# Optimization experiments

Hardware: AMD Instinct MI355X
Metric: run time of the kernel (lower is better)

Reference implementation:

```python
import jax, jax.numpy as jnp
import numpy as np

N_USERS = 100_000
N_ITEMS = 50_000
N_NODES = N_USERS + N_ITEMS      # 150_000
EMB_DIM = 64
N_EDGES = 2_400_000              # avg degree ~16
N_LAYERS = 3
S_TEMP = 1.0                     # config['s_temp']


def segment_softmax(logits, seg, n):
    # numerically stable scatter-softmax over groups defined by seg
    m = jax.ops.segment_max(logits, seg, num_segments=n)
    e = jnp.exp(logits - m[seg])
    s = jax.ops.segment_sum(e, seg, num_segments=n)
    return e / s[seg]


def setup_inputs() -> dict:
    key = jax.random.key(0)
    k1, k2, k3 = jax.random.split(key, 3)
    emb_table = jax.random.normal(k1, (N_NODES, EMB_DIM), dtype=jnp.float32) * 0.1
    edge_index = jax.random.randint(k2, (2, N_EDGES), 0, N_NODES, dtype=jnp.int64)
    edge_attrs = jax.random.normal(k3, (N_EDGES,), dtype=jnp.float32)
    return {"emb_table": emb_table, "edge_index": edge_index, "edge_attrs": edge_attrs}


def reference(emb_table, edge_index, edge_attrs):
    frm, to = edge_index[0], edge_index[1]
    # DySimGCF edge normalization: geometric mean of incoming/outgoing scatter-softmax
    incoming = segment_softmax(edge_attrs / S_TEMP, to, N_NODES)
    outgoing = segment_softmax(edge_attrs / S_TEMP, frm, N_NODES)
    norm = jnp.sqrt(incoming * outgoing)          # [E]

    x = emb_table                                  # [N, D]
    embs = [x]
    for _ in range(N_LAYERS):
        # message = norm * x_j ; aggregate 'add' at destination == sparse mm
        msg = norm[:, None] * x[frm]               # [E, D]
        x = jax.ops.segment_sum(msg, to, num_segments=N_NODES)
        embs.append(x)
    # layer-average (lightGCN-style readout)
    out = jnp.mean(jnp.stack(embs, axis=1), axis=1)  # [N, D]
    return out
```

## Files before the change

### kernel.cpp

```cpp
#include <hip/hip_runtime.h>
#include <hip/hip_bf16.h>

#define N_NODES 150000
#define N_EDGES 2400000
#define DIM     64
#define MAXDEG  64

#define NB      256
#define NPB     587
#define NSHARD  4
#define CAPS    2816
#define BINBLK  512
#define BINTHR  512
#define EPB     ((N_EDGES + BINBLK - 1) / BINBLK)

__device__ __forceinline__ unsigned enc14(float v) {
    unsigned b = __float_as_uint(v);
    b += (1u << 13);
    int e5 = (int)((b >> 23) & 0xFF) - 104;
    if (e5 <= 0) return 0u;
    if (e5 > 31) e5 = 31;
    return ((unsigned)e5 << 9) | ((b >> 14) & 0x1FFu);
}
__device__ __forceinline__ float dec14(unsigned w) {
    return __uint_as_float((w << 14) + (104u << 23));
}
__device__ __forceinline__ unsigned packbf(float a, float b) {
    unsigned ua = __float_as_uint(a), ub = __float_as_uint(b);
    ua += 0x7FFFu + ((ua >> 16) & 1u);
    ub += 0x7FFFu + ((ub >> 16) & 1u);
    return (ua >> 16) | (ub & 0xFFFF0000u);
}
__device__ __forceinline__ float bflo(unsigned v) { return __uint_as_float(v << 16); }
__device__ __forceinline__ float bfhi(unsigned v) { return __uint_as_float(v & 0xFFFF0000u); }

__device__ __forceinline__ void scanNB(unsigned* scanBuf, int tid) {
    for (int off = 1; off < NB; off <<= 1) {
        unsigned v = 0u;
        if (tid < NB) { v = scanBuf[tid]; if (tid >= off) v += scanBuf[tid - off]; }
        __syncthreads();
        if (tid < NB) scanBuf[tid] = v;
        __syncthreads();
    }
}

__global__ __launch_bounds__(BINTHR) void binA_kernel(const float* __restrict__ attrs,
                                                      const int* __restrict__ frm,
                                                      const int* __restrict__ to,
                                                      unsigned* __restrict__ gcntT,
                                                      unsigned* __restrict__ gcntF,
                                                      uint2* __restrict__ recT,
                                                      unsigned* __restrict__ recF) {
    __shared__ unsigned hist[NB], baseL[NB], gBase[NB], cur[NB], scanBuf[NB];
    __shared__ uint2 bufT[EPB];
    unsigned* bufF = (unsigned*)bufT;

    int tid = threadIdx.x;
    int e0 = blockIdx.x * EPB;
    int e1 = e0 + EPB; if (e1 > N_EDGES) e1 = N_EDGES;
    int n = e1 - e0;
    unsigned shard = blockIdx.x & (NSHARD - 1);

    for (int i = tid; i < NB; i += BINTHR) { hist[i] = 0u; cur[i] = 0u; }
    __syncthreads();
    for (int e = e0 + tid; e < e1; e += BINTHR)
        atomicAdd(&hist[(unsigned)to[e] / NPB], 1u);
    __syncthreads();
    if (tid < NB) scanBuf[tid] = hist[tid];
    __syncthreads();
    scanNB(scanBuf, tid);
    if (tid < NB) {
        baseL[tid] = scanBuf[tid] - hist[tid];
        gBase[tid] = hist[tid] ? atomicAdd(&gcntT[tid * NSHARD + shard], hist[tid]) : 0u;
    }
    __syncthreads();
    for (int e = e0 + tid; e < e1; e += BINTHR) {
        unsigned t = (unsigned)to[e], f = (unsigned)frm[e];
        unsigned v14 = enc14(expf(attrs[e]));
        unsigned b = t / NPB;
        unsigned pos = baseL[b] + atomicAdd(&cur[b], 1u);
        bufT[pos] = make_uint2((t << 14) | v14, f);
    }
    __syncthreads();
    for (int s = tid; s < n; s += BINTHR) {
        uint2 r = bufT[s];
        unsigned b = (r.x >> 14) / NPB;
        unsigned dst = gBase[b] + ((unsigned)s - baseL[b]);
        if (dst < CAPS) recT[(size_t)(b * NSHARD + shard) * CAPS + dst] = r;
    }
    __syncthreads();

    for (int i = tid; i < NB; i += BINTHR) { hist[i] = 0u; cur[i] = 0u; }
    __syncthreads();
    for (int e = e0 + tid; e < e1; e += BINTHR)
        atomicAdd(&hist[(unsigned)frm[e] / NPB], 1u);
    __syncthreads();
    if (tid < NB) scanBuf[tid] = hist[tid];
    __syncthreads();
    scanNB(scanBuf, tid);
    if (tid < NB) {
        baseL[tid] = scanBuf[tid] - hist[tid];
        gBase[tid] = hist[tid] ? atomicAdd(&gcntF[tid * NSHARD + shard], hist[tid]) : 0u;
    }
    __syncthreads();
    for (int e = e0 + tid; e < e1; e += BINTHR) {
        unsigned f = (unsigned)frm[e];
        unsigned v14 = enc14(expf(attrs[e]));
        unsigned b = f / NPB;
        unsigned pos = baseL[b] + atomicAdd(&cur[b], 1u);
        bufF[pos] = (f << 14) | v14;
    }
    __syncthreads();
    for (int s = tid; s < n; s += BINTHR) {
        unsigned r = bufF[s];
        unsigned b = (r >> 14) / NPB;
        unsigned dst = gBase[b] + ((unsigned)s - baseL[b]);
        if (dst < CAPS) recF[(size_t)(b * NSHARD + shard) * CAPS + dst] = r;
    }
}

__global__ __launch_bounds__(1024) void sumF_kernel(const unsigned* __restrict__ recF,
                                                    const unsigned* __restrict__ gcntF,
                                                    float* __restrict__ s_out) {
    __shared__ float acc[NPB];
    int b = blockIdx.x;
    for (int i = threadIdx.x; i < NPB; i += blockDim.x) acc[i] = 0.f;
    __syncthreads();
    unsigned nodeBase = (unsigned)b * NPB;
    for (int s = 0; s < NSHARD; ++s) {
        unsigned n = gcntF[b * NSHARD + s];
        if (n > CAPS) n = CAPS;
        const unsigned* r = recF + (size_t)(b * NSHARD + s) * CAPS;
        for (unsigned i = threadIdx.x; i < n; i += blockDim.x) {
            unsigned w = r[i];
            atomicAdd(&acc[(w >> 14) - nodeBase], dec14(w & 0x3FFFu));
        }
    }
    __syncthreads();
    for (int i = threadIdx.x; i < NPB && (int)nodeBase + i < N_NODES; i += blockDim.x)
        s_out[nodeBase + i] = acc[i];
}

__global__ __launch_bounds__(1024) void buildT_kernel(const uint2* __restrict__ recT,
                                                      const unsigned* __restrict__ gcntT,
                                                      const float* __restrict__ s_out,
                                                      unsigned* __restrict__ edges,
                                                      int* __restrict__ fill) {
    __shared__ float    sinL[NPB];
    __shared__ unsigned filL[NPB];
    int b = blockIdx.x;
    for (int i = threadIdx.x; i < NPB; i += blockDim.x) { sinL[i] = 0.f; filL[i] = 0u; }
    __syncthreads();
    unsigned nodeBase = (unsigned)b * NPB;
    for (int s = 0; s < NSHARD; ++s) {
        unsigned n = gcntT[b * NSHARD + s];
        if (n > CAPS) n = CAPS;
        const uint2* r = recT + (size_t)(b * NSHARD + s) * CAPS;
        for (unsigned i = threadIdx.x; i < n; i += blockDim.x) {
            uint2 w = r[i];
            atomicAdd(&sinL[(w.x >> 14) - nodeBase], dec14(w.x & 0x3FFFu));
        }
    }
    __syncthreads();
    for (int s = 0; s < NSHARD; ++s) {
        unsigned n = gcntT[b * NSHARD + s];
        if (n > CAPS) n = CAPS;
        const uint2* r = recT + (size_t)(b * NSHARD + s) * CAPS;
        for (unsigned i = threadIdx.x; i < n; i += blockDim.x) {
            uint2 w = r[i];
            unsigned t = w.x >> 14;
            float ea = dec14(w.x & 0x3FFFu);
            unsigned f = w.y;
            float nrm = ea * rsqrtf(sinL[t - nodeBase] * s_out[f]);
            unsigned p = atomicAdd(&filL[t - nodeBase], 1u);
            if (p < MAXDEG) edges[(size_t)t * MAXDEG + p] = (f << 14) | enc14(nrm);
        }
    }
    __syncthreads();
    for (int i = threadIdx.x; i < NPB && (int)nodeBase + i < N_NODES; i += blockDim.x) {
        unsigned n = filL[i]; if (n > MAXDEG) n = MAXDEG;
        unsigned n8 = (n + 7u) & ~7u; if (n8 > MAXDEG) n8 = MAXDEG;
        for (unsigned p = n; p < n8; ++p)
            edges[(size_t)(nodeBase + i) * MAXDEG + p] = 0u;
        fill[nodeBase + i] = (int)n8;
    }
}

__global__ __launch_bounds__(256) void cvt_kernel(const float* __restrict__ emb,
                                                  unsigned* __restrict__ embB) {
    int i = blockIdx.x * blockDim.x + threadIdx.x;
    if (i >= N_NODES * DIM / 4) return;
    float4 v = reinterpret_cast<const float4*>(emb)[i];
    uint2 p;
    p.x = packbf(v.x, v.y);
    p.y = packbf(v.z, v.w);
    reinterpret_cast<uint2*>(embB)[i] = p;
}

#define EFMA(W, X) { float n_ = dec14((W) & 0x3FFFu); \
                     accx += n_ * bflo(X); accy += n_ * bfhi(X); }

template<bool FIRST, bool WRITE_Y>
__global__ __launch_bounds__(256) void layer_kernel(const unsigned* __restrict__ xw,
                                                    const float* __restrict__ emb,
                                                    const unsigned* __restrict__ edges,
                                                    const int* __restrict__ fill,
                                                    unsigned* __restrict__ yw,
                                                    float* __restrict__ out) {
    int node = blockIdx.x * 4 + (threadIdx.x >> 6);
    if (node >= N_NODES) return;
    int lane = threadIdx.x & 63;
    int cnt = fill[node];
    unsigned w = edges[(size_t)node * MAXDEG + lane];
    int half = lane >> 5;
    int p    = lane & 31;
    float accx = 0.f, accy = 0.f;
    if (cnt > 0) {
        unsigned wa = (unsigned)__shfl((int)w, 0 + half, 64);
        unsigned wb = (unsigned)__shfl((int)w, 2 + half, 64);
        unsigned wc = (unsigned)__shfl((int)w, 4 + half, 64);
        unsigned wd = (unsigned)__shfl((int)w, 6 + half, 64);
        unsigned xa = xw[(wa >> 14) * 32 + p];
        unsigned xb = xw[(wb >> 14) * 32 + p];
        unsigned xc = xw[(wc >> 14) * 32 + p];
        unsigned xd = xw[(wd >> 14) * 32 + p];
        for (int j = 8; j < cnt; j += 8) {
            unsigned we = (unsigned)__shfl((int)w, j +     half, 64);
            unsigned wf = (unsigned)__shfl((int)w, j + 2 + half, 64);
            unsigned wg = (unsigned)__shfl((int)w, j + 4 + half, 64);
            unsigned wh = (unsigned)__shfl((int)w, j + 6 + half, 64);
            unsigned xe = xw[(we >> 14) * 32 + p];
            unsigned xf = xw[(wf >> 14) * 32 + p];
            unsigned xg = xw[(wg >> 14) * 32 + p];
            unsigned xh = xw[(wh >> 14) * 32 + p];
            EFMA(wa, xa); EFMA(wb, xb); EFMA(wc, xc); EFMA(wd, xd);
            wa = we; wb = wf; wc = wg; wd = wh;
            xa = xe; xb = xf; xc = xg; xd = xh;
        }
        EFMA(wa, xa); EFMA(wb, xb); EFMA(wc, xc); EFMA(wd, xd);
    }
    accx += __shfl_xor(accx, 32, 64);
    accy += __shfl_xor(accy, 32, 64);
    if (lane < 32) {
        if (WRITE_Y) yw[node * 32 + p] = packbf(accx, accy);
        float2* o2 = reinterpret_cast<float2*>(out + (size_t)node * DIM) + p;
        if (FIRST) {
            float2 e2 = reinterpret_cast<const float2*>(emb + (size_t)node * DIM)[p];
            *o2 = make_float2(0.25f * (e2.x + accx), 0.25f * (e2.y + accy));
        } else {
            float2 o = *o2;
            o.x += 0.25f * accx;
            o.y += 0.25f * accy;
            *o2 = o;
        }
    }
}

extern "C" void kernel_launch(void* const* d_in, const int* in_sizes, int n_in,
                              void* d_out, int out_size, void* d_ws, size_t ws_size,
                              hipStream_t stream) {
    const float* emb   = (const float*)d_in[0];
    const int*   eidx  = (const int*)d_in[1];
    const float* attrs = (const float*)d_in[2];
    const int* frm = eidx;
    const int* to  = eidx + N_EDGES;
    float* out = (float*)d_out;

    float*    s_out = (float*)d_ws;
    int*      fill  = (int*)(s_out + N_NODES);
    unsigned* gcntT = (unsigned*)(fill + N_NODES);
    unsigned* gcntF = gcntT + NB * NSHARD;
    unsigned* edges = gcntF + NB * NSHARD;
    unsigned* embB  = edges + (size_t)N_NODES * MAXDEG;
    unsigned* U     = embB + (size_t)N_NODES * 32;
    uint2*    recT  = (uint2*)U;
    unsigned* recF  = (unsigned*)(recT + (size_t)NB * NSHARD * CAPS);
    unsigned* xA    = U;
    unsigned* xB    = xA + (size_t)N_NODES * 32;

    const int B = 256;
    const int gV4 = (N_NODES * DIM / 4 + B - 1) / B;
    const int gN  = (N_NODES + 3) / 4;

    hipMemsetAsync(gcntT, 0, 2 * NB * NSHARD * sizeof(unsigned), stream);
    binA_kernel<<<BINBLK, BINTHR, 0, stream>>>(attrs, frm, to, gcntT, gcntF, recT, recF);
    sumF_kernel<<<NB, 1024, 0, stream>>>(recF, gcntF, s_out);
    buildT_kernel<<<NB, 1024, 0, stream>>>(recT, gcntT, s_out, edges, fill);
    cvt_kernel<<<gV4, B, 0, stream>>>(emb, embB);

    layer_kernel<true,  true ><<<gN, B, 0, stream>>>(embB, emb, edges, fill, xA, out);
    layer_kernel<false, true ><<<gN, B, 0, stream>>>(xA,   emb, edges, fill, xB, out);
    layer_kernel<false, false><<<gN, B, 0, stream>>>(xB,   emb, edges, fill, xA, out);
}
```

Before: 287.8 us.

## Gather uint2 rows per quarter-wave and defer layer-average to final layer

The layer kernel now has each 16-lane quarter-wave gather a full 64-dim bf16 row as uint2, so each 8-edge step covers two edges per quarter. Edge words are read directly as uint4 per lane group instead of being broadcast with shuffles, followed by a two-stage cross-quarter reduction. The per-layer read-modify-write of the fp32 output is removed: intermediate layers only write bf16 x, and the final layer sums the bf16 embedding, x1, x2 and its own result. This cuts output memory traffic and shuffle work. The cost is that the readout now uses the bf16-rounded input embedding instead of fp32, which slightly reduces accuracy.

Result: faster. 262.3 us (-8.9%).

```diff
diff --git a/kernel.cpp b/kernel.cpp
--- a/kernel.cpp
+++ b/kernel.cpp
@@ -197,61 +197,64 @@
     reinterpret_cast<uint2*>(embB)[i] = p;
 }
 
-#define EFMA(W, X) { float n_ = dec14((W) & 0x3FFFu); \
-                     accx += n_ * bflo(X); accy += n_ * bfhi(X); }
-
-template<bool FIRST, bool WRITE_Y>
-__global__ __launch_bounds__(256) void layer_kernel(const unsigned* __restrict__ xw,
-                                                    const float* __restrict__ emb,
+#define QSEL(W, V4) { unsigned t1_ = (q & 1) ? (V4).y : (V4).x; \
+                      unsigned t2_ = (q & 1) ? (V4).w : (V4).z; \
+                      W = (q & 2) ? t2_ : t1_; }
+#define QFMA(N, X) { ax += (N) * bflo((X).x); ay += (N) * bfhi((X).x); \
+                     az += (N) * bflo((X).y); aw_ += (N) * bfhi((X).y); }
+
+template<bool FINAL>
+__global__ __launch_bounds__(256) void layer_kernel(const uint2* __restrict__ xw2,
                                                     const unsigned* __restrict__ edges,
                                                     const int* __restrict__ fill,
-                                                    unsigned* __restrict__ yw,
+                                                    uint2* __restrict__ yw2,
+                                                    const uint2* __restrict__ embB2,
+                                                    const uint2* __restrict__ x1w2,
+                                                    const uint2* __restrict__ x2w2,
                                                     float* __restrict__ out) {
     int node = blockIdx.x * 4 + (threadIdx.x >> 6);
-    if (node >= N_NODES) return;
+    int nodeU = __builtin_amdgcn_readfirstlane(node);
     int lane = threadIdx.x & 63;
-    int cnt = fill[node];
-    unsigned w = edges[(size_t)node * MAXDEG + lane];
-    int half = lane >> 5;
-    int p    = lane & 31;
-    float accx = 0.f, accy = 0.f;
+    int q  = lane >> 4;
+    int p4 = lane & 15;
+    int cnt = fill[nodeU];
+    const uint4* erow4 = reinterpret_cast<const uint4*>(edges + (size_t)nodeU * MAXDEG);
+    float ax = 0.f, ay = 0.f, az = 0.f, aw_ = 0.f;
     if (cnt > 0) {
-        unsigned wa = (unsigned)__shfl((int)w, 0 + half, 64);
-        unsigned wb = (unsigned)__shfl((int)w, 2 + half, 64);
-        unsigned wc = (unsigned)__shfl((int)w, 4 + half, 64);
-        unsigned wd = (unsigned)__shfl((int)w, 6 + half, 64);
-        unsigned xa = xw[(wa >> 14) * 32 + p];
-        unsigned xb = xw[(wb >> 14) * 32 + p];
-        unsigned xc = xw[(wc >> 14) * 32 + p];
-        unsigned xd = xw[(wd >> 14) * 32 + p];
+        uint4 A = erow4[0], B = erow4[1];
+        unsigned w0, w1;
+        QSEL(w0, A); QSEL(w1, B);
+        uint2 xa = xw2[(w0 >> 14) * 16 + p4];
+        uint2 xb = xw2[(w1 >> 14) * 16 + p4];
+        float n0 = dec14(w0 & 0x3FFFu), n1 = dec14(w1 & 0x3FFFu);
         for (int j = 8; j < cnt; j += 8) {
-            unsigned we = (unsigned)__shfl((int)w, j +     half, 64);
-            unsigned wf = (unsigned)__shfl((int)w, j + 2 + half, 64);
-            unsigned wg = (unsigned)__shfl((int)w, j + 4 + half, 64);
-            unsigned wh = (unsigned)__shfl((int)w, j + 6 + half, 64);
-            unsigned xe = xw[(we >> 14) * 32 + p];
-            unsigned xf = xw[(wf >> 14) * 32 + p];
-            unsigned xg = xw[(wg >> 14) * 32 + p];
-            unsigned xh = xw[(wh >> 14) * 32 + p];
-            EFMA(wa, xa); EFMA(wb, xb); EFMA(wc, xc); EFMA(wd, xd);
-            wa = we; wb = wf; wc = wg; wd = wh;
-            xa = xe; xb = xf; xc = xg; xd = xh;
-        }
-        EFMA(wa, xa); EFMA(wb, xb); EFMA(wc, xc); EFMA(wd, xd);
-    }
-    accx += __shfl_xor(accx, 32, 64);
-    accy += __shfl_xor(accy, 32, 64);
-    if (lane < 32) {
-        if (WRITE_Y) yw[node * 32 + p] = packbf(accx, accy);
-        float2* o2 = reinterpret_cast<float2*>(out + (size_t)node * DIM) + p;
-        if (FIRST) {
-            float2 e2 = reinterpret_cast<const float2*>(emb + (size_t)node * DIM)[p];
-            *o2 = make_float2(0.25f * (e2.x + accx), 0.25f * (e2.y + accy));
+            uint4 A1 = erow4[j >> 2], B1 = erow4[(j >> 2) + 1];
+            unsigned v0, v1;
+            QSEL(v0, A1); QSEL(v1, B1);
+            uint2 xc = xw2[(v0 >> 14) * 16 + p4];
+            uint2 xd = xw2[(v1 >> 14) * 16 + p4];
+            float m0 = dec14(v0 & 0x3FFFu), m1 = dec14(v1 & 0x3FFFu);
+            QFMA(n0, xa); QFMA(n1, xb);
+            n0 = m0; n1 = m1; xa = xc; xb = xd;
+        }
+        QFMA(n0, xa); QFMA(n1, xb);
+    }
+    ax += __shfl_xor(ax, 16, 64); ay += __shfl_xor(ay, 16, 64);
+    az += __shfl_xor(az, 16, 64); aw_ += __shfl_xor(aw_, 16, 64);
+    ax += __shfl_xor(ax, 32, 64); ay += __shfl_xor(ay, 32, 64);
+    az += __shfl_xor(az, 32, 64); aw_ += __shfl_xor(aw_, 32, 64);
+    if (lane < 16) {
+        int o = nodeU * 16 + p4;
+        if (!FINAL) {
+            yw2[o] = make_uint2(packbf(ax, ay), packbf(az, aw_));
         } else {
-            float2 o = *o2;
-            o.x += 0.25f * accx;
-            o.y += 0.25f * accy;
-            *o2 = o;
+            uint2 e = embB2[o], u1 = x1w2[o], u2 = x2w2[o];
+            float4 r;
+            r.x = 0.25f * (bflo(e.x) + bflo(u1.x) + bflo(u2.x) + ax);
+            r.y = 0.25f * (bfhi(e.x) + bfhi(u1.x) + bfhi(u2.x) + ay);
+            r.z = 0.25f * (bflo(e.y) + bflo(u1.y) + bflo(u2.y) + az);
+            r.w = 0.25f * (bfhi(e.y) + bfhi(u1.y) + bfhi(u2.y) + aw_);
+            reinterpret_cast<float4*>(out)[o] = r;
         }
     }
 }
@@ -280,7 +283,7 @@
 
     const int B = 256;
     const int gV4 = (N_NODES * DIM / 4 + B - 1) / B;
-    const int gN  = (N_NODES + 3) / 4;
+    const int gN  = N_NODES / 4;
 
     hipMemsetAsync(gcntT, 0, 2 * NB * NSHARD * sizeof(unsigned), stream);
     binA_kernel<<<BINBLK, BINTHR, 0, stream>>>(attrs, frm, to, gcntT, gcntF, recT, recF);
@@ -288,7 +291,14 @@
     buildT_kernel<<<NB, 1024, 0, stream>>>(recT, gcntT, s_out, edges, fill);
     cvt_kernel<<<gV4, B, 0, stream>>>(emb, embB);
 
-    layer_kernel<true,  true ><<<gN, B, 0, stream>>>(embB, emb, edges, fill, xA, out);
-    layer_kernel<false, true ><<<gN, B, 0, stream>>>(xA,   emb, edges, fill, xB, out);
-    layer_kernel<false, false><<<gN, B, 0, stream>>>(xB,   emb, edges, fill, xA, out);
-}
+    const uint2* embB2 = (const uint2*)embB;
+    uint2* xA2 = (uint2*)xA;
+    uint2* xB2 = (uint2*)xB;
+
+    layer_kernel<false><<<gN, B, 0, stream>>>(embB2, edges, fill, xA2,
+                                              embB2, xA2, xB2, out);
+    layer_kernel<false><<<gN, B, 0, stream>>>((const uint2*)xA, edges, fill, xB2,
+                                              embB2, xA2, xB2, out);
+    layer_kernel<true ><<<gN, B, 0, stream>>>((const uint2*)xB, edges, fill, xA2,
+                                              embB2, xA2, xB2, out);
+}
```
